# Kernel tuning notes

Measured on AMD Instinct MI355X. Metric: run time of the kernel, lower is better.

The kernel has to match this reference:

```python
import jax, jax.numpy as jnp
import numpy as np

D_MODEL = 1024
N_HEADS = 16
D_HEAD = 64
B, S = 8, 1024
EPS = 1.1920929e-07  # torch.finfo(float32).eps, RMSNorm default eps=None


def setup_inputs() -> dict:
    key = jax.random.key(0)
    k1, k2, k3 = jax.random.split(key, 3)
    x = jax.random.normal(k1, (B, S, D_MODEL), dtype=jnp.float32)
    W_qkv = jax.random.normal(k2, (3 * N_HEADS * D_HEAD, D_MODEL), dtype=jnp.float32) * 0.02
    b_qkv = jnp.zeros((3 * N_HEADS * D_HEAD,), dtype=jnp.float32)
    W_o = jax.random.normal(k3, (D_MODEL, N_HEADS * D_HEAD), dtype=jnp.float32) * 0.02
    b_o = jnp.zeros((D_MODEL,), dtype=jnp.float32)
    return {"x": x, "W_qkv": W_qkv, "b_qkv": b_qkv, "W_o": W_o, "b_o": b_o}


def reference(x, W_qkv, b_qkv, W_o, b_o):
    # RMSNorm, no affine
    normed = x * jax.lax.rsqrt(jnp.mean(x * x, axis=-1, keepdims=True) + EPS)
    qkv = normed @ W_qkv.T + b_qkv                       # [b, s, 3*H*Dh]
    # packing order '(n_heads d_head n_qkv)' -> reshape (H, Dh, 3), unbind last
    qkv = qkv.reshape(*qkv.shape[:-1], N_HEADS, D_HEAD, 3)
    q, k, v = qkv[..., 0], qkv[..., 1], qkv[..., 2]       # [b, s, H, Dh]
    scores = jnp.einsum('bqhd,bkhd->bhqk', q, k)          # no 1/sqrt(d) scaling
    seq = x.shape[-2]
    causal_mask = jnp.triu(jnp.ones((seq, seq), dtype=bool), k=1)  # True above diag
    scores = jnp.where(causal_mask, -jnp.inf, scores)
    # NOTE: softmax over the QUERY axis (dim=-2), faithful to the source
    attn = jax.nn.softmax(scores, axis=-2)                # [b, h, q, k]
    z = jnp.einsum('bhqk,bkhd->bqhd', attn, v)            # [b, q, H, Dh]
    z = z.reshape(*z.shape[:-2], N_HEADS * D_HEAD)
    return z @ W_o.T + b_o
```

## Files before the change

kernel.cpp:

```cpp
#include <hip/hip_runtime.h>
#include <hip/hip_bf16.h>

typedef _Float16 f16;
typedef _Float16 f16x8 __attribute__((ext_vector_type(8)));
typedef _Float16 f16x4 __attribute__((ext_vector_type(4)));
typedef float f32x4 __attribute__((ext_vector_type(4)));

constexpr int Bb = 8, Ss = 1024, Hh = 16, DH = 64, DM = 1024, N3 = 3072;
constexpr int Mm = Bb * Ss;
constexpr float EPS = 1.1920929e-07f;

__device__ __forceinline__ void gll16(const f16* g, f16* l) {
    __builtin_amdgcn_global_load_lds(
        (__attribute__((address_space(1))) void*)(g),
        (__attribute__((address_space(3))) void*)(l), 16, 0, 0);
}

__global__ void rmscast_kernel(const float* __restrict__ x, f16* __restrict__ xh) {
    const int row = blockIdx.x;
    const int t = threadIdx.x;
    float4 v = *(const float4*)(x + (size_t)row * DM + t * 4);
    float s = v.x * v.x + v.y * v.y + v.z * v.z + v.w * v.w;
#pragma unroll
    for (int o = 32; o > 0; o >>= 1) s += __shfl_down(s, o, 64);
    __shared__ float red[4];
    if ((t & 63) == 0) red[t >> 6] = s;
    __syncthreads();
    float tot = red[0] + red[1] + red[2] + red[3];
    float sc = rsqrtf(tot * (1.0f / DM) + EPS);
    f16x4 hv = {(f16)(v.x * sc), (f16)(v.y * sc), (f16)(v.z * sc), (f16)(v.w * sc)};
    *(f16x4*)(xh + (size_t)row * DM + t * 4) = hv;
}

__global__ void castw_kernel(const float* __restrict__ Wqkv, const float* __restrict__ Wo,
                             f16* __restrict__ wq, f16* __restrict__ wo) {
    int i = blockIdx.x * 256 + threadIdx.x;
    const int n1 = (N3 * DM) / 4;
    if (i < n1) {
        float4 v = ((const float4*)Wqkv)[i];
        f16x4 h = {(f16)v.x, (f16)v.y, (f16)v.z, (f16)v.w};
        ((f16x4*)wq)[i] = h;
    } else {
        int j = i - n1;
        float4 v = ((const float4*)Wo)[j];
        f16x4 h = {(f16)v.x, (f16)v.y, (f16)v.z, (f16)v.w};
        ((f16x4*)wo)[j] = h;
    }
}

__launch_bounds__(256, 2)
__global__ void qkv_gemm(const f16* __restrict__ xh, const f16* __restrict__ wq,
                         const float* __restrict__ bqkv, f16* __restrict__ qk,
                         f16* __restrict__ vT) {
    __shared__ __align__(16) f16 As[128 * 64];
    __shared__ __align__(16) f16 Bs[128 * 64];
    const int t = threadIdx.x, lane = t & 63, w = t >> 6;
    const int gm0 = blockIdx.y * 128, gn0 = blockIdx.x * 128;
    const int wm = (w >> 1) * 64, wn = (w & 1) * 64;
    const int srow = lane >> 3, sslot = (lane & 7) ^ srow;
    const int r15 = lane & 15, cs = lane >> 4;

    const f16* Ag = xh + (size_t)(gm0 + srow) * DM + sslot * 8;
    const f16* Bg = wq + (size_t)(gn0 + srow) * DM + sslot * 8;

    int aoff[4][2], boff[4][2];
#pragma unroll
    for (int i = 0; i < 4; ++i) {
        int Ra = wm + i * 16 + r15;
        aoff[i][0] = Ra * 64 + ((cs ^ (Ra & 7)) * 8);
        aoff[i][1] = Ra * 64 + (((cs + 4) ^ (Ra & 7)) * 8);
        int Rb = wn + i * 16 + r15;
        boff[i][0] = Rb * 64 + ((cs ^ (Rb & 7)) * 8);
        boff[i][1] = Rb * 64 + (((cs + 4) ^ (Rb & 7)) * 8);
    }
    f32x4 acc[4][4] = {};

    for (int k0 = 0; k0 < DM; k0 += 64) {
        __syncthreads();
#pragma unroll
        for (int j = 0; j < 4; ++j) {
            int c = w * 4 + j;
            gll16(Ag + (size_t)c * 8 * DM + k0, As + c * 512);
            gll16(Bg + (size_t)c * 8 * DM + k0, Bs + c * 512);
        }
        __syncthreads();
#pragma unroll
        for (int half = 0; half < 2; ++half) {
            f16x8 af[4], bf[4];
#pragma unroll
            for (int i = 0; i < 4; ++i) af[i] = *(const f16x8*)&As[aoff[i][half]];
#pragma unroll
            for (int i = 0; i < 4; ++i) bf[i] = *(const f16x8*)&Bs[boff[i][half]];
#pragma unroll
            for (int mi = 0; mi < 4; ++mi)
#pragma unroll
                for (int ni = 0; ni < 4; ++ni)
                    acc[mi][ni] = __builtin_amdgcn_mfma_f32_16x16x32_f16(af[mi], bf[ni], acc[mi][ni], 0, 0, 0);
        }
    }
#pragma unroll
    for (int mi = 0; mi < 4; ++mi) {
#pragma unroll
        for (int ni = 0; ni < 4; ++ni) {
            int jcol = gn0 + wn + ni * 16 + r15;
            float bb = bqkv[jcol];
            int h = jcol / 192, r = jcol % 192;
            int d = r / 3, which = r % 3;
            int m0 = gm0 + wm + mi * 16 + cs * 4;
            int b = m0 >> 10, s0 = m0 & 1023;
            int bh = b * Hh + h;
            if (which == 2) {
                f16x4 pv = {(f16)(acc[mi][ni][0] + bb), (f16)(acc[mi][ni][1] + bb),
                            (f16)(acc[mi][ni][2] + bb), (f16)(acc[mi][ni][3] + bb)};
                *(f16x4*)(vT + ((size_t)bh * DH + d) * Ss + s0) = pv;
            } else {
                size_t base = ((size_t)which * (Bb * Hh) + bh) * (size_t)(Ss * DH) + (size_t)s0 * DH + d;
#pragma unroll
                for (int jj = 0; jj < 4; ++jj)
                    qk[base + (size_t)jj * DH] = (f16)(acc[mi][ni][jj] + bb);
            }
        }
    }
}

__launch_bounds__(512, 2)
__global__ void colstats_kernel(const f16* __restrict__ qk, float* __restrict__ cbuf) {
    __shared__ __align__(16) f16 KsA[128 * 64];
    __shared__ __align__(16) f16 KsB[128 * 64];
    __shared__ __align__(16) f16 Qs[2][64 * 64];
    const int t = threadIdx.x, lane = t & 63, w = t >> 6;
    const int r15 = lane & 15, cs = lane >> 4;
    const int srow = lane >> 3, sslot = (lane & 7) ^ srow;
    const int bh = blockIdx.y, si = blockIdx.x;
    const int kA0 = si * 128, kB0 = (7 - si) * 128;
    const size_t hs = (size_t)(Bb * Hh) * (Ss * DH);
    const f16* qb = qk + (size_t)bh * (Ss * DH);
    const f16* kb = qb + hs;
    const int qt0 = 2 * si;

    gll16(kb + (size_t)(kA0 + w * 16 + srow) * DH + sslot * 8, KsA + (2 * w) * 512);
    gll16(kb + (size_t)(kA0 + w * 16 + 8 + srow) * DH + sslot * 8, KsA + (2 * w + 1) * 512);
    gll16(kb + (size_t)(kB0 + w * 16 + srow) * DH + sslot * 8, KsB + (2 * w) * 512);
    gll16(kb + (size_t)(kB0 + w * 16 + 8 + srow) * DH + sslot * 8, KsB + (2 * w + 1) * 512);
    gll16(qb + (size_t)(qt0 * 64 + w * 8 + srow) * DH + sslot * 8, Qs[0] + w * 512);
    __syncthreads();
    const int Rk = w * 16 + r15;
    f16x8 kfA0 = *(const f16x8*)&KsA[Rk * 64 + ((cs ^ (Rk & 7)) * 8)];
    f16x8 kfA1 = *(const f16x8*)&KsA[Rk * 64 + (((cs + 4) ^ (Rk & 7)) * 8)];
    f16x8 kfB0 = *(const f16x8*)&KsB[Rk * 64 + ((cs ^ (Rk & 7)) * 8)];
    f16x8 kfB1 = *(const f16x8*)&KsB[Rk * 64 + (((cs + 4) ^ (Rk & 7)) * 8)];
    const int kwA = kA0 + w * 16, kglobA = kwA + r15;
    const int kwB = kB0 + w * 16, kglobB = kwB + r15;
    float la = 0.0f, lb = 0.0f;
    int cur = 0;

    for (int qt = qt0; qt < 16; ++qt) {
        if (qt + 1 < 16)
            gll16(qb + (size_t)((qt + 1) * 64 + w * 8 + srow) * DH + sslot * 8,
                  Qs[cur ^ 1] + w * 512);
        const bool engA = (qt * 64 + 63 >= kwA);
        const bool engB = (qt * 64 + 63 >= kwB);
        if (engA || engB) {
#pragma unroll
            for (int qs = 0; qs < 4; ++qs) {
                const int qb16 = qt * 64 + qs * 16;
                const bool nA = engA && (qb16 + 15 >= kwA);
                const bool nB = engB && (qb16 + 15 >= kwB);
                if (!(nA || nB)) continue;
                int Ra = qs * 16 + r15;
                f16x8 a0 = *(const f16x8*)&Qs[cur][Ra * 64 + ((cs ^ (Ra & 7)) * 8)];
                f16x8 a1 = *(const f16x8*)&Qs[cur][Ra * 64 + (((cs + 4) ^ (Ra & 7)) * 8)];
                if (nA) {
                    f32x4 sf = {};
                    sf = __builtin_amdgcn_mfma_f32_16x16x32_f16(a0, kfA0, sf, 0, 0, 0);
                    sf = __builtin_amdgcn_mfma_f32_16x16x32_f16(a1, kfA1, sf, 0, 0, 0);
#pragma unroll
                    for (int j = 0; j < 4; ++j) {
                        int q = qb16 + cs * 4 + j;
                        la += (q >= kglobA) ? __expf(sf[j]) : 0.0f;
                    }
                }
                if (nB) {
                    f32x4 sf = {};
                    sf = __builtin_amdgcn_mfma_f32_16x16x32_f16(a0, kfB0, sf, 0, 0, 0);
                    sf = __builtin_amdgcn_mfma_f32_16x16x32_f16(a1, kfB1, sf, 0, 0, 0);
#pragma unroll
                    for (int j = 0; j < 4; ++j) {
                        int q = qb16 + cs * 4 + j;
                        lb += (q >= kglobB) ? __expf(sf[j]) : 0.0f;
                    }
                }
            }
        }
        __syncthreads();
        cur ^= 1;
    }
    la += __shfl_xor(la, 16, 64);
    la += __shfl_xor(la, 32, 64);
    lb += __shfl_xor(lb, 16, 64);
    lb += __shfl_xor(lb, 32, 64);
    if (cs == 0) {
        cbuf[bh * Ss + kglobA] = logf(la);
        cbuf[bh * Ss + kglobB] = logf(lb);
    }
}

__launch_bounds__(512, 2)
__global__ void attnz_kernel(const f16* __restrict__ qk, const f16* __restrict__ vT,
                             const float* __restrict__ cbuf, f16* __restrict__ z) {
    __shared__ __align__(16) f16 QsA[128 * 64];
    __shared__ __align__(16) f16 QsB[128 * 64];
    __shared__ __align__(16) f16 Ks[64 * 64];
    __shared__ __align__(16) f16 Vs[64 * 64];
    __shared__ __align__(16) float cb[1024];
    const int t = threadIdx.x, lane = t & 63, w = t >> 6;
    const int r15 = lane & 15, cs = lane >> 4;
    const int srow = lane >> 3, sslot = (lane & 7) ^ srow;
    const int bh = blockIdx.y, si = blockIdx.x;
    const int qtA = si, qtB = 7 - si;
    const size_t hs = (size_t)(Bb * Hh) * (Ss * DH);
    const f16* qb = qk + (size_t)bh * (Ss * DH);
    const f16* kb = qb + hs;
    const f16* vb = vT + (size_t)bh * (DH * Ss);

    gll16(qb + (size_t)(qtA * 128 + w * 16 + srow) * DH + sslot * 8, QsA + (2 * w) * 512);
    gll16(qb + (size_t)(qtA * 128 + w * 16 + 8 + srow) * DH + sslot * 8, QsA + (2 * w + 1) * 512);
    gll16(qb + (size_t)(qtB * 128 + w * 16 + srow) * DH + sslot * 8, QsB + (2 * w) * 512);
    gll16(qb + (size_t)(qtB * 128 + w * 16 + 8 + srow) * DH + sslot * 8, QsB + (2 * w + 1) * 512);
    gll16(kb + (size_t)(w * 8 + srow) * DH + sslot * 8, Ks + w * 512);
    gll16(vb + (size_t)(w * 8 + srow) * Ss + sslot * 8, Vs + w * 512);
    {
        float2 c2 = *(const float2*)(cbuf + bh * Ss + t * 2);
        *(float2*)&cb[t * 2] = c2;
    }
    __syncthreads();
    const int Rq = w * 16 + r15;
    f16x8 aqA0 = *(const f16x8*)&QsA[Rq * 64 + ((cs ^ (Rq & 7)) * 8)];
    f16x8 aqA1 = *(const f16x8*)&QsA[Rq * 64 + (((cs + 4) ^ (Rq & 7)) * 8)];
    f16x8 aqB0 = *(const f16x8*)&QsB[Rq * 64 + ((cs ^ (Rq & 7)) * 8)];
    f16x8 aqB1 = *(const f16x8*)&QsB[Rq * 64 + (((cs + 4) ^ (Rq & 7)) * 8)];
    f32x4 accA[4] = {}, accB[4] = {};
    const int qwA = qtA * 128 + w * 16, qA = qwA + r15;
    const int qwB = qtB * 128 + w * 16, qB = qwB + r15;
    const int nktA = 2 * qtA + 2, nktB = 2 * qtB + 2;
    const int sAl = ((cs & 1) * 2) * 16 + r15;
    const int sBl = sAl + 16;
    const bool hi = (cs >> 1) != 0;

    for (int kt = 0; kt < nktB; ++kt) {
        if (kt) {
            __syncthreads();
            gll16(kb + (size_t)(kt * 64 + w * 8 + srow) * DH + sslot * 8, Ks + w * 512);
            gll16(vb + (size_t)(w * 8 + srow) * Ss + kt * 64 + sslot * 8, Vs + w * 512);
            __syncthreads();
        }
        const int kb0 = kt * 64;
        const bool doA = (kt < nktA) && (kb0 <= qwA + 15);
        const bool doB = (kb0 <= qwB + 15);
        if (!(doA || doB)) continue;

        unsigned pkA[4][2], pkB[4][2];
#pragma unroll
        for (int tl = 0; tl < 4; ++tl) {
            const int kbase = kb0 + tl * 16;
            const bool nA = doA && (kbase <= qwA + 15);
            const bool nB = doB && (kbase <= qwB + 15);
            pkA[tl][0] = 0u; pkA[tl][1] = 0u;
            pkB[tl][0] = 0u; pkB[tl][1] = 0u;
            if (!(nA || nB)) continue;
            int Rk2 = tl * 16 + r15;
            f16x8 kf0 = *(const f16x8*)&Ks[Rk2 * 64 + ((cs ^ (Rk2 & 7)) * 8)];
            f16x8 kf1 = *(const f16x8*)&Ks[Rk2 * 64 + (((cs + 4) ^ (Rk2 & 7)) * 8)];
            f32x4 cv = *(const f32x4*)&cb[kbase + cs * 4];
            if (nA) {
                f32x4 sf = {};
                sf = __builtin_amdgcn_mfma_f32_16x16x32_f16(kf0, aqA0, sf, 0, 0, 0);
                sf = __builtin_amdgcn_mfma_f32_16x16x32_f16(kf1, aqA1, sf, 0, 0, 0);
                f16 p[4];
#pragma unroll
                for (int j = 0; j < 4; ++j) {
                    int k = kbase + cs * 4 + j;
                    p[j] = (f16)((k <= qA) ? __expf(sf[j] - cv[j]) : 0.0f);
                }
                union { f16 h[2]; unsigned u; } u0, u1;
                u0.h[0] = p[0]; u0.h[1] = p[1];
                u1.h[0] = p[2]; u1.h[1] = p[3];
                pkA[tl][0] = u0.u; pkA[tl][1] = u1.u;
            }
            if (nB) {
                f32x4 sf = {};
                sf = __builtin_amdgcn_mfma_f32_16x16x32_f16(kf0, aqB0, sf, 0, 0, 0);
                sf = __builtin_amdgcn_mfma_f32_16x16x32_f16(kf1, aqB1, sf, 0, 0, 0);
                f16 p[4];
#pragma unroll
                for (int j = 0; j < 4; ++j) {
                    int k = kbase + cs * 4 + j;
                    p[j] = (f16)((k <= qB) ? __expf(sf[j] - cv[j]) : 0.0f);
                }
                union { f16 h[2]; unsigned u; } u0, u1;
                u0.h[0] = p[0]; u0.h[1] = p[1];
                u1.h[0] = p[2]; u1.h[1] = p[3];
                pkB[tl][0] = u0.u; pkB[tl][1] = u1.u;
            }
        }
        f16x8 bfA[2], bfB[2];
        bool uA[2], uB[2];
#pragma unroll
        for (int c = 0; c < 2; ++c) {
            uA[c] = doA && (kb0 + c * 32 <= qwA + 15);
            uB[c] = doB && (kb0 + c * 32 <= qwB + 15);
            if (uA[c]) {
                unsigned a0 = (unsigned)__shfl((int)pkA[2 * c][0], sAl, 64);
                unsigned a1 = (unsigned)__shfl((int)pkA[2 * c][1], sAl, 64);
                unsigned a2 = (unsigned)__shfl((int)pkA[2 * c][0], sBl, 64);
                unsigned a3 = (unsigned)__shfl((int)pkA[2 * c][1], sBl, 64);
                unsigned b0_ = (unsigned)__shfl((int)pkA[2 * c + 1][0], sAl, 64);
                unsigned b1_ = (unsigned)__shfl((int)pkA[2 * c + 1][1], sAl, 64);
                unsigned b2_ = (unsigned)__shfl((int)pkA[2 * c + 1][0], sBl, 64);
                unsigned b3_ = (unsigned)__shfl((int)pkA[2 * c + 1][1], sBl, 64);
                union { unsigned u[4]; f16x8 v; } bf;
                bf.u[0] = hi ? b0_ : a0;
                bf.u[1] = hi ? b1_ : a1;
                bf.u[2] = hi ? b2_ : a2;
                bf.u[3] = hi ? b3_ : a3;
                bfA[c] = bf.v;
            }
            if (uB[c]) {
                unsigned a0 = (unsigned)__shfl((int)pkB[2 * c][0], sAl, 64);
                unsigned a1 = (unsigned)__shfl((int)pkB[2 * c][1], sAl, 64);
                unsigned a2 = (unsigned)__shfl((int)pkB[2 * c][0], sBl, 64);
                unsigned a3 = (unsigned)__shfl((int)pkB[2 * c][1], sBl, 64);
                unsigned b0_ = (unsigned)__shfl((int)pkB[2 * c + 1][0], sAl, 64);
                unsigned b1_ = (unsigned)__shfl((int)pkB[2 * c + 1][1], sAl, 64);
                unsigned b2_ = (unsigned)__shfl((int)pkB[2 * c + 1][0], sBl, 64);
                unsigned b3_ = (unsigned)__shfl((int)pkB[2 * c + 1][1], sBl, 64);
                union { unsigned u[4]; f16x8 v; } bf;
                bf.u[0] = hi ? b0_ : a0;
                bf.u[1] = hi ? b1_ : a1;
                bf.u[2] = hi ? b2_ : a2;
                bf.u[3] = hi ? b3_ : a3;
                bfB[c] = bf.v;
            }
        }
#pragma unroll
        for (int dt = 0; dt < 4; ++dt) {
            int Rv = dt * 16 + r15;
            f16x8 v0 = *(const f16x8*)&Vs[Rv * 64 + ((cs ^ (Rv & 7)) * 8)];
            f16x8 v1 = *(const f16x8*)&Vs[Rv * 64 + (((4 + cs) ^ (Rv & 7)) * 8)];
            if (uA[0]) accA[dt] = __builtin_amdgcn_mfma_f32_16x16x32_f16(v0, bfA[0], accA[dt], 0, 0, 0);
            if (uA[1]) accA[dt] = __builtin_amdgcn_mfma_f32_16x16x32_f16(v1, bfA[1], accA[dt], 0, 0, 0);
            if (uB[0]) accB[dt] = __builtin_amdgcn_mfma_f32_16x16x32_f16(v0, bfB[0], accB[dt], 0, 0, 0);
            if (uB[1]) accB[dt] = __builtin_amdgcn_mfma_f32_16x16x32_f16(v1, bfB[1], accB[dt], 0, 0, 0);
        }
    }
    const int b = bh >> 4, h = bh & 15;
#pragma unroll
    for (int dt = 0; dt < 4; ++dt) {
        f16x4 zvA = {(f16)accA[dt][0], (f16)accA[dt][1], (f16)accA[dt][2], (f16)accA[dt][3]};
        *(f16x4*)(z + ((size_t)(b * Ss + qA)) * DM + h * DH + dt * 16 + cs * 4) = zvA;
        f16x4 zvB = {(f16)accB[dt][0], (f16)accB[dt][1], (f16)accB[dt][2], (f16)accB[dt][3]};
        *(f16x4*)(z + ((size_t)(b * Ss + qB)) * DM + h * DH + dt * 16 + cs * 4) = zvB;
    }
}

__launch_bounds__(256, 2)
__global__ void out_gemm(const f16* __restrict__ z, const f16* __restrict__ wo,
                         const float* __restrict__ bo, float* __restrict__ out) {
    __shared__ __align__(16) f16 As[128 * 64];
    __shared__ __align__(16) f16 Bs[128 * 64];
    const int t = threadIdx.x, lane = t & 63, w = t >> 6;
    const int gm0 = blockIdx.y * 128, gn0 = blockIdx.x * 128;
    const int wm = (w >> 1) * 64, wn = (w & 1) * 64;
    const int srow = lane >> 3, sslot = (lane & 7) ^ srow;
    const int r15 = lane & 15, cs = lane >> 4;

    const f16* Ag = z + (size_t)(gm0 + srow) * DM + sslot * 8;
    const f16* Bg = wo + (size_t)(gn0 + srow) * DM + sslot * 8;

    int aoff[4][2], boff[4][2];
#pragma unroll
    for (int i = 0; i < 4; ++i) {
        int Ra = wm + i * 16 + r15;
        aoff[i][0] = Ra * 64 + ((cs ^ (Ra & 7)) * 8);
        aoff[i][1] = Ra * 64 + (((cs + 4) ^ (Ra & 7)) * 8);
        int Rb = wn + i * 16 + r15;
        boff[i][0] = Rb * 64 + ((cs ^ (Rb & 7)) * 8);
        boff[i][1] = Rb * 64 + (((cs + 4) ^ (Rb & 7)) * 8);
    }
    f32x4 acc[4][4] = {};

    for (int k0 = 0; k0 < DM; k0 += 64) {
        __syncthreads();
#pragma unroll
        for (int j = 0; j < 4; ++j) {
            int c = w * 4 + j;
            gll16(Ag + (size_t)c * 8 * DM + k0, As + c * 512);
            gll16(Bg + (size_t)c * 8 * DM + k0, Bs + c * 512);
        }
        __syncthreads();
#pragma unroll
        for (int half = 0; half < 2; ++half) {
            f16x8 af[4], bf[4];
#pragma unroll
            for (int i = 0; i < 4; ++i) af[i] = *(const f16x8*)&As[aoff[i][half]];
#pragma unroll
            for (int i = 0; i < 4; ++i) bf[i] = *(const f16x8*)&Bs[boff[i][half]];
#pragma unroll
            for (int mi = 0; mi < 4; ++mi)
#pragma unroll
                for (int ni = 0; ni < 4; ++ni)
                    acc[mi][ni] = __builtin_amdgcn_mfma_f32_16x16x32_f16(af[mi], bf[ni], acc[mi][ni], 0, 0, 0);
        }
    }
#pragma unroll
    for (int mi = 0; mi < 4; ++mi) {
#pragma unroll
        for (int ni = 0; ni < 4; ++ni) {
            int n = gn0 + wn + ni * 16 + r15;
            float bb = bo[n];
#pragma unroll
            for (int jj = 0; jj < 4; ++jj) {
                int m = gm0 + wm + mi * 16 + cs * 4 + jj;
                out[(size_t)m * DM + n] = acc[mi][ni][jj] + bb;
            }
        }
    }
}

extern "C" void kernel_launch(void* const* d_in, const int* in_sizes, int n_in,
                              void* d_out, int out_size, void* d_ws, size_t ws_size,
                              hipStream_t stream) {
    (void)in_sizes; (void)n_in; (void)out_size; (void)ws_size;
    const float* x    = (const float*)d_in[0];
    const float* Wqkv = (const float*)d_in[1];
    const float* bqkv = (const float*)d_in[2];
    const float* Wo   = (const float*)d_in[3];
    const float* bo   = (const float*)d_in[4];
    float* out = (float*)d_out;

    char* ws = (char*)d_ws;
    f16* xh   = (f16*)ws;
    f16* z    = (f16*)ws;
    f16* wq   = (f16*)(ws + 16777216);
    f16* wo   = (f16*)(ws + 23068672);
    f16* qk   = (f16*)(ws + 25165824);
    f16* vT   = (f16*)(ws + 58720256);
    float* cbuf = (float*)(ws + 75497472);

    rmscast_kernel<<<Mm, 256, 0, stream>>>(x, xh);
    castw_kernel<<<(N3 * DM + DM * DM) / 1024, 256, 0, stream>>>(Wqkv, Wo, wq, wo);
    qkv_gemm<<<dim3(N3 / 128, Mm / 128), 256, 0, stream>>>(xh, wq, bqkv, qk, vT);
    colstats_kernel<<<dim3(4, Bb * Hh), 512, 0, stream>>>(qk, cbuf);
    attnz_kernel<<<dim3(4, Bb * Hh), 512, 0, stream>>>(qk, vT, cbuf, z);
    out_gemm<<<dim3(DM / 128, Mm / 128), 256, 0, stream>>>(z, wo, bo, out);
}
```

Measured before the change: 202.1 us.

## Merge prep kernels, swizzle GEMM block order, load resident Q/K fragments directly

Fuses the RMSNorm cast and the weight cast into one launch. Remaps the GEMM block indices so that consecutive blocks land on different XCD-interleaved tiles, aiming for better L2 reuse. In colstats and attnz, the per-wave resident K or Q fragments are now loaded straight from global memory into registers instead of being staged through LDS. This cuts LDS usage, which may raise occupancy, at the cost of uncoalesced 16-byte global reads.

```diff
diff --git a/kernel.cpp b/kernel.cpp
--- a/kernel.cpp
+++ b/kernel.cpp
@@ -16,35 +16,36 @@
         (__attribute__((address_space(3))) void*)(l), 16, 0, 0);
 }
 
-__global__ void rmscast_kernel(const float* __restrict__ x, f16* __restrict__ xh) {
-    const int row = blockIdx.x;
+__global__ void prep_kernel(const float* __restrict__ x, f16* __restrict__ xh,
+                            const float* __restrict__ Wqkv, const float* __restrict__ Wo,
+                            f16* __restrict__ wq, f16* __restrict__ wo) {
     const int t = threadIdx.x;
-    float4 v = *(const float4*)(x + (size_t)row * DM + t * 4);
-    float s = v.x * v.x + v.y * v.y + v.z * v.z + v.w * v.w;
-#pragma unroll
-    for (int o = 32; o > 0; o >>= 1) s += __shfl_down(s, o, 64);
-    __shared__ float red[4];
-    if ((t & 63) == 0) red[t >> 6] = s;
-    __syncthreads();
-    float tot = red[0] + red[1] + red[2] + red[3];
-    float sc = rsqrtf(tot * (1.0f / DM) + EPS);
-    f16x4 hv = {(f16)(v.x * sc), (f16)(v.y * sc), (f16)(v.z * sc), (f16)(v.w * sc)};
-    *(f16x4*)(xh + (size_t)row * DM + t * 4) = hv;
-}
-
-__global__ void castw_kernel(const float* __restrict__ Wqkv, const float* __restrict__ Wo,
-                             f16* __restrict__ wq, f16* __restrict__ wo) {
-    int i = blockIdx.x * 256 + threadIdx.x;
-    const int n1 = (N3 * DM) / 4;
-    if (i < n1) {
-        float4 v = ((const float4*)Wqkv)[i];
-        f16x4 h = {(f16)v.x, (f16)v.y, (f16)v.z, (f16)v.w};
-        ((f16x4*)wq)[i] = h;
+    if (blockIdx.x < Mm) {
+        const int row = blockIdx.x;
+        float4 v = *(const float4*)(x + (size_t)row * DM + t * 4);
+        float s = v.x * v.x + v.y * v.y + v.z * v.z + v.w * v.w;
+#pragma unroll
+        for (int o = 32; o > 0; o >>= 1) s += __shfl_down(s, o, 64);
+        __shared__ float red[4];
+        if ((t & 63) == 0) red[t >> 6] = s;
+        __syncthreads();
+        float tot = red[0] + red[1] + red[2] + red[3];
+        float sc = rsqrtf(tot * (1.0f / DM) + EPS);
+        f16x4 hv = {(f16)(v.x * sc), (f16)(v.y * sc), (f16)(v.z * sc), (f16)(v.w * sc)};
+        *(f16x4*)(xh + (size_t)row * DM + t * 4) = hv;
     } else {
-        int j = i - n1;
-        float4 v = ((const float4*)Wo)[j];
-        f16x4 h = {(f16)v.x, (f16)v.y, (f16)v.z, (f16)v.w};
-        ((f16x4*)wo)[j] = h;
+        int i = (blockIdx.x - Mm) * 256 + t;
+        const int n1 = (N3 * DM) / 4;
+        if (i < n1) {
+            float4 v = ((const float4*)Wqkv)[i];
+            f16x4 h = {(f16)v.x, (f16)v.y, (f16)v.z, (f16)v.w};
+            ((f16x4*)wq)[i] = h;
+        } else {
+            int j = i - n1;
+            float4 v = ((const float4*)Wo)[j];
+            f16x4 h = {(f16)v.x, (f16)v.y, (f16)v.z, (f16)v.w};
+            ((f16x4*)wo)[j] = h;
+        }
     }
 }
 
@@ -55,7 +56,9 @@
     __shared__ __align__(16) f16 As[128 * 64];
     __shared__ __align__(16) f16 Bs[128 * 64];
     const int t = threadIdx.x, lane = t & 63, w = t >> 6;
-    const int gm0 = blockIdx.y * 128, gn0 = blockIdx.x * 128;
+    const int bid = blockIdx.y * gridDim.x + blockIdx.x;
+    const int swz = (bid & 7) * 192 + (bid >> 3);
+    const int gm0 = (swz / 24) * 128, gn0 = (swz % 24) * 128;
     const int wm = (w >> 1) * 64, wn = (w & 1) * 64;
     const int srow = lane >> 3, sslot = (lane & 7) ^ srow;
     const int r15 = lane & 15, cs = lane >> 4;
@@ -125,8 +128,6 @@
 
 __launch_bounds__(512, 2)
 __global__ void colstats_kernel(const f16* __restrict__ qk, float* __restrict__ cbuf) {
-    __shared__ __align__(16) f16 KsA[128 * 64];
-    __shared__ __align__(16) f16 KsB[128 * 64];
     __shared__ __align__(16) f16 Qs[2][64 * 64];
     const int t = threadIdx.x, lane = t & 63, w = t >> 6;
     const int r15 = lane & 15, cs = lane >> 4;
@@ -138,19 +139,15 @@
     const f16* kb = qb + hs;
     const int qt0 = 2 * si;
 
-    gll16(kb + (size_t)(kA0 + w * 16 + srow) * DH + sslot * 8, KsA + (2 * w) * 512);
-    gll16(kb + (size_t)(kA0 + w * 16 + 8 + srow) * DH + sslot * 8, KsA + (2 * w + 1) * 512);
-    gll16(kb + (size_t)(kB0 + w * 16 + srow) * DH + sslot * 8, KsB + (2 * w) * 512);
-    gll16(kb + (size_t)(kB0 + w * 16 + 8 + srow) * DH + sslot * 8, KsB + (2 * w + 1) * 512);
+    const int kwA = kA0 + w * 16, kglobA = kwA + r15;
+    const int kwB = kB0 + w * 16, kglobB = kwB + r15;
+    f16x8 kfA0 = *(const f16x8*)(kb + (size_t)(kwA + r15) * DH + cs * 8);
+    f16x8 kfA1 = *(const f16x8*)(kb + (size_t)(kwA + r15) * DH + 32 + cs * 8);
+    f16x8 kfB0 = *(const f16x8*)(kb + (size_t)(kwB + r15) * DH + cs * 8);
+    f16x8 kfB1 = *(const f16x8*)(kb + (size_t)(kwB + r15) * DH + 32 + cs * 8);
+
     gll16(qb + (size_t)(qt0 * 64 + w * 8 + srow) * DH + sslot * 8, Qs[0] + w * 512);
     __syncthreads();
-    const int Rk = w * 16 + r15;
-    f16x8 kfA0 = *(const f16x8*)&KsA[Rk * 64 + ((cs ^ (Rk & 7)) * 8)];
-    f16x8 kfA1 = *(const f16x8*)&KsA[Rk * 64 + (((cs + 4) ^ (Rk & 7)) * 8)];
-    f16x8 kfB0 = *(const f16x8*)&KsB[Rk * 64 + ((cs ^ (Rk & 7)) * 8)];
-    f16x8 kfB1 = *(const f16x8*)&KsB[Rk * 64 + (((cs + 4) ^ (Rk & 7)) * 8)];
-    const int kwA = kA0 + w * 16, kglobA = kwA + r15;
-    const int kwB = kB0 + w * 16, kglobB = kwB + r15;
     float la = 0.0f, lb = 0.0f;
     int cur = 0;
 
@@ -208,8 +205,6 @@
 __launch_bounds__(512, 2)
 __global__ void attnz_kernel(const f16* __restrict__ qk, const f16* __restrict__ vT,
                              const float* __restrict__ cbuf, f16* __restrict__ z) {
-    __shared__ __align__(16) f16 QsA[128 * 64];
-    __shared__ __align__(16) f16 QsB[128 * 64];
     __shared__ __align__(16) f16 Ks[64 * 64];
     __shared__ __align__(16) f16 Vs[64 * 64];
     __shared__ __align__(16) float cb[1024];
@@ -223,10 +218,13 @@
     const f16* kb = qb + hs;
     const f16* vb = vT + (size_t)bh * (DH * Ss);
 
-    gll16(qb + (size_t)(qtA * 128 + w * 16 + srow) * DH + sslot * 8, QsA + (2 * w) * 512);
-    gll16(qb + (size_t)(qtA * 128 + w * 16 + 8 + srow) * DH + sslot * 8, QsA + (2 * w + 1) * 512);
-    gll16(qb + (size_t)(qtB * 128 + w * 16 + srow) * DH + sslot * 8, QsB + (2 * w) * 512);
-    gll16(qb + (size_t)(qtB * 128 + w * 16 + 8 + srow) * DH + sslot * 8, QsB + (2 * w + 1) * 512);
+    const int qwA = qtA * 128 + w * 16, qA = qwA + r15;
+    const int qwB = qtB * 128 + w * 16, qB = qwB + r15;
+    f16x8 aqA0 = *(const f16x8*)(qb + (size_t)(qwA + r15) * DH + cs * 8);
+    f16x8 aqA1 = *(const f16x8*)(qb + (size_t)(qwA + r15) * DH + 32 + cs * 8);
+    f16x8 aqB0 = *(const f16x8*)(qb + (size_t)(qwB + r15) * DH + cs * 8);
+    f16x8 aqB1 = *(const f16x8*)(qb + (size_t)(qwB + r15) * DH + 32 + cs * 8);
+
     gll16(kb + (size_t)(w * 8 + srow) * DH + sslot * 8, Ks + w * 512);
     gll16(vb + (size_t)(w * 8 + srow) * Ss + sslot * 8, Vs + w * 512);
     {
@@ -234,14 +232,7 @@
         *(float2*)&cb[t * 2] = c2;
     }
     __syncthreads();
-    const int Rq = w * 16 + r15;
-    f16x8 aqA0 = *(const f16x8*)&QsA[Rq * 64 + ((cs ^ (Rq & 7)) * 8)];
-    f16x8 aqA1 = *(const f16x8*)&QsA[Rq * 64 + (((cs + 4) ^ (Rq & 7)) * 8)];
-    f16x8 aqB0 = *(const f16x8*)&QsB[Rq * 64 + ((cs ^ (Rq & 7)) * 8)];
-    f16x8 aqB1 = *(const f16x8*)&QsB[Rq * 64 + (((cs + 4) ^ (Rq & 7)) * 8)];
     f32x4 accA[4] = {}, accB[4] = {};
-    const int qwA = qtA * 128 + w * 16, qA = qwA + r15;
-    const int qwB = qtB * 128 + w * 16, qB = qwB + r15;
     const int nktA = 2 * qtA + 2, nktB = 2 * qtB + 2;
     const int sAl = ((cs & 1) * 2) * 16 + r15;
     const int sBl = sAl + 16;
@@ -369,7 +360,9 @@
     __shared__ __align__(16) f16 As[128 * 64];
     __shared__ __align__(16) f16 Bs[128 * 64];
     const int t = threadIdx.x, lane = t & 63, w = t >> 6;
-    const int gm0 = blockIdx.y * 128, gn0 = blockIdx.x * 128;
+    const int bid = blockIdx.y * gridDim.x + blockIdx.x;
+    const int swz = (bid & 7) * 64 + (bid >> 3);
+    const int gm0 = (swz / 8) * 128, gn0 = (swz % 8) * 128;
     const int wm = (w >> 1) * 64, wn = (w & 1) * 64;
     const int srow = lane >> 3, sslot = (lane & 7) ^ srow;
     const int r15 = lane & 15, cs = lane >> 4;
@@ -447,8 +440,7 @@
     f16* vT   = (f16*)(ws + 58720256);
     float* cbuf = (float*)(ws + 75497472);
 
-    rmscast_kernel<<<Mm, 256, 0, stream>>>(x, xh);
-    castw_kernel<<<(N3 * DM + DM * DM) / 1024, 256, 0, stream>>>(Wqkv, Wo, wq, wo);
+    prep_kernel<<<Mm + 4096, 256, 0, stream>>>(x, xh, Wqkv, Wo, wq, wo);
     qkv_gemm<<<dim3(N3 / 128, Mm / 128), 256, 0, stream>>>(xh, wq, bqkv, qk, vT);
     colstats_kernel<<<dim3(4, Bb * Hh), 512, 0, stream>>>(qk, cbuf);
     attnz_kernel<<<dim3(4, Bb * Hh), 512, 0, stream>>>(qk, vT, cbuf, z);
```

After: 196.2 us. 1.03x faster.
